# Kernel tuning notes

Hardware: AMD Instinct MI355X
Metric: run time of the kernel (lower is better)

Reference implementation:

```python
import jax, jax.numpy as jnp
import numpy as np


def setup_inputs() -> dict:
    key = jax.random.key(0)
    k1, k2 = jax.random.split(key)
    n_points = 32768
    n_elements = 2048
    # evaluation points in [0, 1)
    x_eval = jax.random.uniform(k1, (n_points, 1), dtype=jnp.float32)
    # sorted node coordinates (monotone 1D mesh on [0, 1))
    x_full = jnp.sort(jax.random.uniform(k2, (n_elements + 1,), dtype=jnp.float32))
    return {"x_eval": x_eval, "x_full": x_full}


def reference(x_eval, x_full):
    # Vectorized over all elements at once (original loops in Python per element).
    # xa = x_full[i], xb = x_full[i+1] for each of the E = n_nodes-1 elements.
    xa = x_full[:-1]                      # [E]
    xb = x_full[1:]                       # [E]
    h = xb - xa                           # [E]
    # layer1 = relu(-x + xb); layer2 = relu(-layer1/(h+eps) + 1)
    layer1 = jax.nn.relu(xb[None, :] - x_eval)            # [P, E] (x_eval is [P,1])
    layer2 = jax.nn.relu(1.0 - layer1 / (h[None, :] + 1e-9))  # [P, E]
    N0_tilde = 1.0 - layer2               # [P, E]  (w3=-1, b3=1)
    N1_tilde = layer2                     # [P, E]  (w3=+1, b3=0)
    first = N0_tilde[:, 0:1]              # [P, 1]
    last = N1_tilde[:, -1:]               # [P, 1]
    n_nodes = x_full.shape[0]
    if n_nodes > 2:
        internal = N0_tilde[:, 1:] + N1_tilde[:, :-1] - 1.0  # [P, E-1]
        return jnp.concatenate([first, internal, last], axis=1)  # [P, n_nodes]
    return jnp.concatenate([first, last], axis=1)
```

## Files before the change

### kernel.cpp

```cpp
#include <hip/hip_runtime.h>
#include <stdint.h>


__global__ __launch_bounds__(256) void hat_rows(const float* __restrict__ x_eval,
                                                const float* __restrict__ x_full,
                                                float* __restrict__ out,
                                                int n_points, int n_nodes) {
    extern __shared__ float s_xf[];
    for (int i = threadIdx.x; i < n_nodes; i += blockDim.x) s_xf[i] = x_full[i];
    __syncthreads();

    if (n_nodes < 2) return;

    const int nb = gridDim.x;
    const int rows_per_block = (n_points + nb - 1) / nb;
    int r0 = blockIdx.x * rows_per_block;
    int r1 = r0 + rows_per_block;
    if (r1 > n_points) r1 = n_points;

    const int tid  = threadIdx.x;
    const int emax = n_nodes - 2;

    for (int p = r0; p < r1; ++p) {
        float x = x_eval[p];

        int lo = 0, hi = n_nodes;
        while (lo < hi) {
            int mid = (lo + hi) >> 1;
            if (s_xf[mid] <= x) lo = mid + 1; else hi = mid;
        }
        int e0 = lo - 1;
        e0 = e0 < 0 ? 0 : (e0 > emax ? emax : e0);
        const int e1 = e0 + 1;

        float xa = s_xf[e0];
        float xb = s_xf[e1];
        float l1   = fmaxf(xb - x, 0.0f);
        float frac = fmaxf(1.0f - l1 / (xb - xa + 1e-9f), 0.0f);
        float v0 = 1.0f - frac;
        float v1 = frac;

        float* row = out + (size_t)p * (size_t)n_nodes;

        uintptr_t addr = (uintptr_t)row;
        int h = (int)((-(addr >> 2)) & 3);
        if (h > n_nodes) h = n_nodes;
        int rem  = n_nodes - h;
        int n4   = rem >> 2;
        int tail = rem & 3;
        int ct   = h + (n4 << 2);

        if (tid < h) {
            int c = tid;
            row[c] = (c == e0) ? v0 : (c == e1 ? v1 : 0.0f);
        } else if (tid - h < tail) {
            int c = ct + (tid - h);
            row[c] = (c == e0) ? v0 : (c == e1 ? v1 : 0.0f);
        }

        float4* __restrict__ row4 = (float4*)(row + h);
        for (int i = tid; i < n4; i += 256) {
            int c = h + (i << 2);
            float4 v;
            v.x = (c     == e0) ? v0 : (c     == e1 ? v1 : 0.0f);
            v.y = (c + 1 == e0) ? v0 : (c + 1 == e1 ? v1 : 0.0f);
            v.z = (c + 2 == e0) ? v0 : (c + 2 == e1 ? v1 : 0.0f);
            v.w = (c + 3 == e0) ? v0 : (c + 3 == e1 ? v1 : 0.0f);
            row4[i] = v;
        }
    }
}

extern "C" void kernel_launch(void* const* d_in, const int* in_sizes, int n_in,
                              void* d_out, int out_size, void* d_ws, size_t ws_size,
                              hipStream_t stream) {
    const float* x_eval = (const float*)d_in[0];
    const float* x_full = (const float*)d_in[1];
    float* out = (float*)d_out;

    int n_points = in_sizes[0];
    int n_nodes  = in_sizes[1];

    int block = 256;
    int grid  = 2048;
    if (grid > n_points) grid = n_points;
    size_t smem = (size_t)n_nodes * sizeof(float);
    hat_rows<<<grid, block, smem, stream>>>(x_eval, x_full, out, n_points, n_nodes);
}
```

Measured before the change: 273.5 us.

## Launch one block per row and binary-search node coordinates directly in global memory

Replaces the persistent grid of 2048 blocks that each loop over 16 rows with one block per evaluation point. The shared-memory staging of the node array and its barrier are removed, and the binary search now reads node coordinates from global memory, where they should stay cache-resident. The aim is more blocks in flight for the write-bound output fill and no per-block shared-memory preload cost. In exchange it launches many more blocks, and every thread repeats a dependent chain of global loads for the search.

```diff
diff --git a/kernel.cpp b/kernel.cpp
--- a/kernel.cpp
+++ b/kernel.cpp
@@ -2,72 +2,61 @@
 #include <stdint.h>
 
 
-__global__ __launch_bounds__(256) void hat_rows(const float* __restrict__ x_eval,
-                                                const float* __restrict__ x_full,
-                                                float* __restrict__ out,
-                                                int n_points, int n_nodes) {
-    extern __shared__ float s_xf[];
-    for (int i = threadIdx.x; i < n_nodes; i += blockDim.x) s_xf[i] = x_full[i];
-    __syncthreads();
-
-    if (n_nodes < 2) return;
-
-    const int nb = gridDim.x;
-    const int rows_per_block = (n_points + nb - 1) / nb;
-    int r0 = blockIdx.x * rows_per_block;
-    int r1 = r0 + rows_per_block;
-    if (r1 > n_points) r1 = n_points;
+__global__ __launch_bounds__(256) void hat_row(const float* __restrict__ x_eval,
+                                               const float* __restrict__ x_full,
+                                               float* __restrict__ out,
+                                               int n_points, int n_nodes) {
+    const int p = blockIdx.x;
+    if (p >= n_points || n_nodes < 2) return;
 
     const int tid  = threadIdx.x;
     const int emax = n_nodes - 2;
 
-    for (int p = r0; p < r1; ++p) {
-        float x = x_eval[p];
+    const float x = x_eval[p];
 
-        int lo = 0, hi = n_nodes;
-        while (lo < hi) {
-            int mid = (lo + hi) >> 1;
-            if (s_xf[mid] <= x) lo = mid + 1; else hi = mid;
-        }
-        int e0 = lo - 1;
-        e0 = e0 < 0 ? 0 : (e0 > emax ? emax : e0);
-        const int e1 = e0 + 1;
+    int lo = 0, hi = n_nodes;
+    while (lo < hi) {
+        int mid = (lo + hi) >> 1;
+        if (x_full[mid] <= x) lo = mid + 1; else hi = mid;
+    }
+    int e0 = lo - 1;
+    e0 = e0 < 0 ? 0 : (e0 > emax ? emax : e0);
+    const int e1 = e0 + 1;
 
-        float xa = s_xf[e0];
-        float xb = s_xf[e1];
-        float l1   = fmaxf(xb - x, 0.0f);
-        float frac = fmaxf(1.0f - l1 / (xb - xa + 1e-9f), 0.0f);
-        float v0 = 1.0f - frac;
-        float v1 = frac;
+    const float xa = x_full[e0];
+    const float xb = x_full[e1];
+    const float l1   = fmaxf(xb - x, 0.0f);
+    const float frac = fmaxf(1.0f - l1 / (xb - xa + 1e-9f), 0.0f);
+    const float v0 = 1.0f - frac;
+    const float v1 = frac;
 
-        float* row = out + (size_t)p * (size_t)n_nodes;
+    float* row = out + (size_t)p * (size_t)n_nodes;
 
-        uintptr_t addr = (uintptr_t)row;
-        int h = (int)((-(addr >> 2)) & 3);
-        if (h > n_nodes) h = n_nodes;
-        int rem  = n_nodes - h;
-        int n4   = rem >> 2;
-        int tail = rem & 3;
-        int ct   = h + (n4 << 2);
+    uintptr_t addr = (uintptr_t)row;
+    int h = (int)((-(addr >> 2)) & 3);
+    if (h > n_nodes) h = n_nodes;
+    const int rem  = n_nodes - h;
+    const int n4   = rem >> 2;
+    const int tail = rem & 3;
+    const int ct   = h + (n4 << 2);
 
-        if (tid < h) {
-            int c = tid;
-            row[c] = (c == e0) ? v0 : (c == e1 ? v1 : 0.0f);
-        } else if (tid - h < tail) {
-            int c = ct + (tid - h);
-            row[c] = (c == e0) ? v0 : (c == e1 ? v1 : 0.0f);
-        }
+    if (tid < h) {
+        int c = tid;
+        row[c] = (c == e0) ? v0 : (c == e1 ? v1 : 0.0f);
+    } else if (tid - h < tail) {
+        int c = ct + (tid - h);
+        row[c] = (c == e0) ? v0 : (c == e1 ? v1 : 0.0f);
+    }
 
-        float4* __restrict__ row4 = (float4*)(row + h);
-        for (int i = tid; i < n4; i += 256) {
-            int c = h + (i << 2);
-            float4 v;
-            v.x = (c     == e0) ? v0 : (c     == e1 ? v1 : 0.0f);
-            v.y = (c + 1 == e0) ? v0 : (c + 1 == e1 ? v1 : 0.0f);
-            v.z = (c + 2 == e0) ? v0 : (c + 2 == e1 ? v1 : 0.0f);
-            v.w = (c + 3 == e0) ? v0 : (c + 3 == e1 ? v1 : 0.0f);
-            row4[i] = v;
-        }
+    float4* __restrict__ row4 = (float4*)(row + h);
+    for (int i = tid; i < n4; i += 256) {
+        int c = h + (i << 2);
+        float4 v;
+        v.x = (c     == e0) ? v0 : (c     == e1 ? v1 : 0.0f);
+        v.y = (c + 1 == e0) ? v0 : (c + 1 == e1 ? v1 : 0.0f);
+        v.z = (c + 2 == e0) ? v0 : (c + 2 == e1 ? v1 : 0.0f);
+        v.w = (c + 3 == e0) ? v0 : (c + 3 == e1 ? v1 : 0.0f);
+        row4[i] = v;
     }
 }
 
@@ -82,8 +71,6 @@
     int n_nodes  = in_sizes[1];
 
     int block = 256;
-    int grid  = 2048;
-    if (grid > n_points) grid = n_points;
-    size_t smem = (size_t)n_nodes * sizeof(float);
-    hat_rows<<<grid, block, smem, stream>>>(x_eval, x_full, out, n_points, n_nodes);
+    int grid  = n_points;
+    hat_row<<<grid, block, 0, stream>>>(x_eval, x_full, out, n_points, n_nodes);
 }
```

New measurement: 265.1 us. -3.1%, faster.
